# Performance work log

Hardware: AMD Instinct MI355X
Metric: run time of the kernel (lower is better)

## Reference

```python
import jax, jax.numpy as jnp
import numpy as np

N_NODES = 100000
N_EDGES = 1600000
IN_CH = 48
OUT_CH = 64
K = 2


def setup_inputs() -> dict:
    key = jax.random.key(0)
    k1, k2, k3, k4 = jax.random.split(key, 4)
    x = jax.random.normal(k1, (N_NODES, IN_CH), dtype=jnp.float32)
    edge_index = jax.random.randint(k2, (2, N_EDGES), 0, N_NODES, dtype=jnp.int64)
    W = jax.random.normal(k3, (IN_CH, OUT_CH), dtype=jnp.float32) * (1.0 / np.sqrt(IN_CH))
    b = jax.random.normal(k4, (OUT_CH,), dtype=jnp.float32) * 0.01
    return {"x": x, "edge_index": edge_index, "W": W, "b": b}


def _propagate(x, row, col):
    n = x.shape[0]
    # degree of each node counted over col (destination) indices
    deg = jax.ops.segment_sum(jnp.ones_like(col, dtype=x.dtype), col, num_segments=n)
    deg_inv_sqrt = jnp.where(deg > 0, jax.lax.rsqrt(jnp.where(deg > 0, deg, 1.0)), 0.0)
    norm = deg_inv_sqrt[row] * deg_inv_sqrt[col]  # [E]
    # gather-scale-scatter: out[col] += x[row] * norm
    msgs = x[row] * norm[:, None]  # [E, d]
    return jax.ops.segment_sum(msgs, col, num_segments=n)


def reference(x, edge_index, W, b):
    row, col = edge_index[0], edge_index[1]
    h = x
    for _ in range(K):
        h = _propagate(h, row, col)
    return h @ W + b
```

## Files before the change

kernel.cpp:

```cpp
#include <hip/hip_runtime.h>
#include <hip/hip_bf16.h>
#include <hip/hip_fp16.h>


#define N_NODES 100000
#define N_EDGES 1600000
#define IN_CH 48
#define OUT_CH 64
#define NBUCKETS 392
#define CAP 4608
#define EPB 2048
#define EPR 8
#define NBLK_EDGE 782
#define NBLK_BKT 391
#define RSTRIDE 32

__global__ void bucket_scatter_kernel(const int* __restrict__ row, const int* __restrict__ col,
                                      int* __restrict__ bucketCnt, int* __restrict__ edge_packed) {
    __shared__ int lh[NBUCKETS];
    __shared__ int lbase[NBUCKETS];
    __shared__ int rec[EPB];
    __shared__ unsigned short sbkt[EPB];
    int tid = threadIdx.x;
    int base = blockIdx.x * EPB;
    for (int i = tid; i < NBUCKETS; i += 256) lh[i] = 0;
    __syncthreads();
    #pragma unroll
    for (int k = 0; k < EPR; k++) {
        int e = base + k * 256 + tid;
        if (e < N_EDGES) {
            int c = col[e];
            int bkt = c >> 8;
            rec[k * 256 + tid] = (row[e] << 8) | (c & 255);
            sbkt[k * 256 + tid] = (unsigned short)bkt;
            atomicAdd(&lh[bkt], 1);
        }
    }
    __syncthreads();
    for (int i = tid; i < NBUCKETS; i += 256) {
        int c = lh[i];
        if (c > 0) lbase[i] = i * CAP + atomicAdd(&bucketCnt[i], c);
        lh[i] = 0;
    }
    __syncthreads();
    int total = min(EPB, N_EDGES - base);
    for (int i = tid; i < total; i += 256) {
        int bkt = sbkt[i];
        int p = atomicAdd(&lh[bkt], 1);
        int dst = lbase[bkt] + p;
        if (dst < (bkt + 1) * CAP)
            edge_packed[dst] = rec[i];
    }
}

__global__ void fine_sort_kernel(const int* __restrict__ edge_packed,
                                 const int* __restrict__ bucketCnt,
                                 int* __restrict__ edge_src,
                                 int* __restrict__ deg, int* __restrict__ start,
                                 float* __restrict__ dis, int* __restrict__ binTotal) {
    __shared__ int fh[256];
    __shared__ int cur[256];
    __shared__ int bh[64];
    __shared__ int wsum2[4];
    __shared__ int stage[CAP];
    int b = blockIdx.x;
    int t = threadIdx.x;
    int s0 = b * CAP;
    int n_edges = min(bucketCnt[b], CAP);
    int nodeBase = b << 8;
    if (t < 256) fh[t] = 0;
    if (t < 64) bh[t] = 0;
    __syncthreads();
    for (int j = t; j < n_edges; j += 512) {
        int rc = edge_packed[s0 + j];
        stage[j] = rc;
        atomicAdd(&fh[rc & 255], 1);
    }
    __syncthreads();
    if (t < 256) {
        int c = fh[t];
        int incl = c;
        int sl = t & 63, sw = t >> 6;
        #pragma unroll
        for (int o = 1; o < 64; o <<= 1) {
            int v = __shfl_up(incl, o, 64);
            if (sl >= o) incl += v;
        }
        if (sl == 63) wsum2[sw] = incl;
        __syncthreads();
        int wbase = 0;
        for (int k = 0; k < sw; k++) wbase += wsum2[k];
        incl += wbase;
        int ex = incl - c;
        int node = nodeBase + t;
        bool valid = (node < N_NODES);
        int d = c;
        float dv = (valid && d > 0) ? rsqrtf((float)d) : 0.0f;
        cur[t] = ex;
        if (valid) {
            deg[node] = d;
            start[node] = s0 + ex;
            dis[node] = dv;
            atomicAdd(&bh[min(d, 63)], 1);
        }
    } else {
        __syncthreads();
    }
    __syncthreads();
    for (int j = t; j < n_edges; j += 512) {
        int rc = stage[j];
        int p = atomicAdd(&cur[rc & 255], 1);
        edge_src[s0 + p] = rc >> 8;
    }
    __syncthreads();
    if (t < 64 && bh[t]) atomicAdd(&binTotal[t], bh[t]);
}

__global__ void scale_kernel(const float* __restrict__ x, const float* __restrict__ dis,
                             __half2* __restrict__ xs) {
    int g = blockIdx.x * 32 + (threadIdx.x >> 3);
    int c = (threadIdx.x & 7) * 3;
    float dd = dis[g];
    const float2* px = (const float2*)x + g * 24 + c;
    float2 v0 = px[0], v1 = px[1], v2 = px[2];
    __half2* q = xs + g * RSTRIDE + c;
    q[0] = __floats2half2_rn(v0.x * dd, v0.y * dd);
    q[1] = __floats2half2_rn(v1.x * dd, v1.y * dd);
    q[2] = __floats2half2_rn(v2.x * dd, v2.y * dd);
}

__global__ void order_kernel(const int* __restrict__ deg, const int* __restrict__ start,
                             const float* __restrict__ dis,
                             const int* __restrict__ binTotal, int* __restrict__ binCursor2,
                             int4* __restrict__ nodeinfo, int n) {
    __shared__ int lhist[64];
    __shared__ int lbase[64];
    int t = threadIdx.x;
    int i = blockIdx.x * 256 + t;
    if (t < 64) lhist[t] = 0;
    __syncthreads();
    int bin = 0, myrank = 0, d = 0;
    float dv = 0.0f;
    if (i < n) {
        d = deg[i];
        dv = dis[i];
        bin = min(d, 63);
        myrank = atomicAdd(&lhist[bin], 1);
    }
    __syncthreads();
    if (t < 64) {
        int c = binTotal[t];
        int incl = c;
        #pragma unroll
        for (int o = 1; o < 64; o <<= 1) {
            int v = __shfl_up(incl, o, 64);
            if (t >= o) incl += v;
        }
        int tot = __shfl(incl, 63, 64);
        int S = tot - incl;
        int add = (lhist[t] > 0) ? atomicAdd(&binCursor2[t], lhist[t]) : 0;
        lbase[t] = S + add;
    }
    __syncthreads();
    if (i < n)
        nodeinfo[lbase[bin] + myrank] = make_int4(i, start[i], d, __float_as_int(dv));
}

#define LOAD3(p, v0, v1, v2) { v0 = (p)[0]; v1 = (p)[1]; v2 = (p)[2]; }
#define ACC6(v0, v1, v2) { \
    float2 u0 = __half22float2(v0), u1 = __half22float2(v1), u2 = __half22float2(v2); \
    a0 += u0.x; a1 += u0.y; a2 += u1.x; a3 += u1.y; a4 += u2.x; a5 += u2.y; }
#define ACC6B(v0, v1, v2) { \
    float2 u0 = __half22float2(v0), u1 = __half22float2(v1), u2 = __half22float2(v2); \
    b0 += u0.x; b1 += u0.y; b2 += u1.x; b3 += u1.y; b4 += u2.x; b5 += u2.y; }

#define DECLD(P) __half2 P##00,P##01,P##02,P##10,P##11,P##12,P##20,P##21,P##22,P##30,P##31,P##32
#define DECLS(S) int S##0, S##1, S##2, S##3
#define LOADSRC(S) { S##0 = edge_src[j]; S##1 = edge_src[j+1]; \
                     S##2 = edge_src[j+2]; S##3 = edge_src[j+3]; j += 4; }
#define ISSUED(P, S, basep) { \
    const __half2* q0 = basep + S##0 * RSTRIDE + lane3; \
    const __half2* q1 = basep + S##1 * RSTRIDE + lane3; \
    const __half2* q2 = basep + S##2 * RSTRIDE + lane3; \
    const __half2* q3 = basep + S##3 * RSTRIDE + lane3; \
    P##00 = q0[0]; P##01 = q0[1]; P##02 = q0[2]; \
    P##10 = q1[0]; P##11 = q1[1]; P##12 = q1[2]; \
    P##20 = q2[0]; P##21 = q2[1]; P##22 = q2[2]; \
    P##30 = q3[0]; P##31 = q3[1]; P##32 = q3[2]; }
#define CONSUMED(P) { ACC6(P##00,P##01,P##02); ACC6B(P##10,P##11,P##12); \
                      ACC6(P##20,P##21,P##22); ACC6B(P##30,P##31,P##32); }

#define GATHER_PIPELINE(basep) { \
    int m = (e - s) >> 2; \
    DECLD(A); DECLD(B); \
    DECLS(sa); DECLS(sb); \
    if (m >= 2) { \
        LOADSRC(sa); LOADSRC(sb); \
        ISSUED(A, sa, basep); \
        m -= 2; \
        while (m >= 2) { \
            LOADSRC(sa); \
            ISSUED(B, sb, basep); \
            CONSUMED(A); \
            LOADSRC(sb); \
            ISSUED(A, sa, basep); \
            CONSUMED(B); \
            m -= 2; \
        } \
        if (m == 1) { \
            LOADSRC(sa); \
            ISSUED(B, sb, basep); \
            CONSUMED(A); \
            ISSUED(A, sa, basep); \
            CONSUMED(B); \
            CONSUMED(A); \
        } else { \
            ISSUED(B, sb, basep); \
            CONSUMED(A); \
            CONSUMED(B); \
        } \
    } else if (m == 1) { \
        LOADSRC(sa); \
        ISSUED(A, sa, basep); \
        CONSUMED(A); \
    } \
    for (; j < e; ++j) { \
        const __half2* p0 = basep + edge_src[j] * RSTRIDE + lane3; \
        __half2 v00, v01, v02; \
        LOAD3(p0, v00, v01, v02); \
        ACC6(v00, v01, v02); \
    } \
    a0 += b0; a1 += b1; a2 += b2; a3 += b3; a4 += b4; a5 += b5; }

__global__ void gather1_kernel(const __half2* __restrict__ xs,
                               const int* __restrict__ edge_src,
                               const int4* __restrict__ nodeinfo,
                               __half2* __restrict__ h1) {
    int g = blockIdx.x * 32 + (threadIdx.x >> 3);
    int lane3 = (threadIdx.x & 7) * 3;
    int4 ni = nodeinfo[g];
    int node = ni.x, s = ni.y, e = s + ni.z;
    float dv = __int_as_float(ni.w);
    float a0 = 0, a1 = 0, a2 = 0, a3 = 0, a4 = 0, a5 = 0;
    float b0 = 0, b1 = 0, b2 = 0, b3 = 0, b4 = 0, b5 = 0;
    int j = s;
    GATHER_PIPELINE(xs);
    float sc = dv * dv;
    __half2* q = h1 + node * RSTRIDE + lane3;
    q[0] = __floats2half2_rn(a0 * sc, a1 * sc);
    q[1] = __floats2half2_rn(a2 * sc, a3 * sc);
    q[2] = __floats2half2_rn(a4 * sc, a5 * sc);
}

__global__ void gather2_gemm_kernel(const __half2* __restrict__ h1,
                                    const int* __restrict__ edge_src,
                                    const int4* __restrict__ nodeinfo,
                                    const float* __restrict__ W,
                                    const float* __restrict__ bias,
                                    float* __restrict__ out) {
    __shared__ float sW[IN_CH * OUT_CH];
    __shared__ float sb[OUT_CH];
    __shared__ float sh[32][IN_CH + 1];

    for (int i = threadIdx.x; i < IN_CH * OUT_CH; i += 256) sW[i] = W[i];
    if (threadIdx.x < OUT_CH) sb[threadIdx.x] = bias[threadIdx.x];

    int nl = threadIdx.x >> 3;
    int lane = threadIdx.x & 7;
    int lane3 = lane * 3;
    int g = blockIdx.x * 32 + nl;
    int4 ni = nodeinfo[g];
    int node = ni.x, s = ni.y, e = s + ni.z;
    float dv = __int_as_float(ni.w);

    float a0 = 0, a1 = 0, a2 = 0, a3 = 0, a4 = 0, a5 = 0;
    float b0 = 0, b1 = 0, b2 = 0, b3 = 0, b4 = 0, b5 = 0;
    int j = s;
    GATHER_PIPELINE(h1);
    int c0 = 6 * lane;
    sh[nl][c0 + 0] = a0 * dv;
    sh[nl][c0 + 1] = a1 * dv;
    sh[nl][c0 + 2] = a2 * dv;
    sh[nl][c0 + 3] = a3 * dv;
    sh[nl][c0 + 4] = a4 * dv;
    sh[nl][c0 + 5] = a5 * dv;
    __syncthreads();

    int j0 = lane * 8;
    float acc[8];
    #pragma unroll
    for (int i = 0; i < 8; i++) acc[i] = sb[j0 + i];
    for (int k = 0; k < IN_CH; k++) {
        float s0 = sh[nl][k];
        #pragma unroll
        for (int i = 0; i < 8; i++) acc[i] += s0 * sW[k * OUT_CH + j0 + i];
    }
    float4* o = (float4*)(out + (size_t)node * OUT_CH + j0);
    o[0] = make_float4(acc[0], acc[1], acc[2], acc[3]);
    o[1] = make_float4(acc[4], acc[5], acc[6], acc[7]);
}

extern "C" void kernel_launch(void* const* d_in, const int* in_sizes, int n_in,
                              void* d_out, int out_size, void* d_ws, size_t ws_size,
                              hipStream_t stream) {
    const float* x   = (const float*)d_in[0];
    const int*   ei  = (const int*)d_in[1];
    const float* W   = (const float*)d_in[2];
    const float* b   = (const float*)d_in[3];
    float* out = (float*)d_out;

    const int* row = ei;
    const int* col = ei + N_EDGES;

    int* ws_i = (int*)d_ws;
    int* bucketCnt    = ws_i;
    int* binTotal     = ws_i + 512;
    int* binCursor2   = ws_i + 576;
    int* deg          = ws_i + 1024;
    int* start        = ws_i + 101376;
    float* dis        = (float*)(ws_i + 201728);
    int4* nodeinfo    = (int4*)(ws_i + 302080);
    int* edge_packed  = ws_i + 703488;
    __half2* xs       = (__half2*)(ws_i + 703488);
    int* edge_src     = ws_i + 3903488;
    __half2* h1       = (__half2*)(ws_i + 5709824);

    hipMemsetAsync(d_ws, 0, 640 * sizeof(int), stream);

    bucket_scatter_kernel<<<NBLK_EDGE, 256, 0, stream>>>(row, col, bucketCnt, edge_packed);
    fine_sort_kernel<<<NBLK_BKT, 512, 0, stream>>>(edge_packed, bucketCnt,
                                                   edge_src, deg, start, dis, binTotal);
    scale_kernel<<<N_NODES / 32, 256, 0, stream>>>(x, dis, xs);
    order_kernel<<<(N_NODES + 255) / 256, 256, 0, stream>>>(deg, start, dis, binTotal,
                                                            binCursor2, nodeinfo, N_NODES);

    gather1_kernel<<<N_NODES / 32, 256, 0, stream>>>(xs, edge_src, nodeinfo, h1);
    gather2_gemm_kernel<<<N_NODES / 32, 256, 0, stream>>>(h1, edge_src, nodeinfo, W, b, out);
}
```

Baseline: 206.1 us.

## Locally sort edges by bucket in shared memory before global scatter

The bucket scatter kernel now makes a histogram pass over col, prefix-scans the per-block bucket counts, and places each edge record into a bucket-sorted shared staging array. The final write loop then walks the staging array sequentially, so consecutive threads write to contiguous global positions within each bucket. This replaces the earlier scattered global writes with more coalesced ones. The cost is an extra read of col and one more scan with its barriers.

```diff
diff --git a/kernel.cpp b/kernel.cpp
--- a/kernel.cpp
+++ b/kernel.cpp
@@ -18,12 +18,48 @@
 __global__ void bucket_scatter_kernel(const int* __restrict__ row, const int* __restrict__ col,
                                       int* __restrict__ bucketCnt, int* __restrict__ edge_packed) {
     __shared__ int lh[NBUCKETS];
+    __shared__ int lofs[NBUCKETS];
     __shared__ int lbase[NBUCKETS];
-    __shared__ int rec[EPB];
+    __shared__ int stage[EPB];
     __shared__ unsigned short sbkt[EPB];
+    __shared__ int wsum[4];
     int tid = threadIdx.x;
     int base = blockIdx.x * EPB;
     for (int i = tid; i < NBUCKETS; i += 256) lh[i] = 0;
+    __syncthreads();
+    #pragma unroll
+    for (int k = 0; k < EPR; k++) {
+        int e = base + k * 256 + tid;
+        if (e < N_EDGES) atomicAdd(&lh[col[e] >> 8], 1);
+    }
+    __syncthreads();
+    {
+        int c0 = (tid < 196) ? lh[2 * tid] : 0;
+        int c1 = (tid < 196) ? lh[2 * tid + 1] : 0;
+        int s = c0 + c1;
+        int incl = s;
+        int lane = tid & 63, w = tid >> 6;
+        #pragma unroll
+        for (int o = 1; o < 64; o <<= 1) {
+            int v = __shfl_up(incl, o, 64);
+            if (lane >= o) incl += v;
+        }
+        if (lane == 63) wsum[w] = incl;
+        __syncthreads();
+        int wbase = 0;
+        for (int k = 0; k < w; k++) wbase += wsum[k];
+        int ex = wbase + incl - s;
+        if (tid < 196) {
+            lofs[2 * tid]     = ex;
+            lofs[2 * tid + 1] = ex + c0;
+        }
+    }
+    __syncthreads();
+    for (int i = tid; i < NBUCKETS; i += 256) {
+        int c = lh[i];
+        if (c > 0) lbase[i] = i * CAP + atomicAdd(&bucketCnt[i], c);
+        lh[i] = 0;
+    }
     __syncthreads();
     #pragma unroll
     for (int k = 0; k < EPR; k++) {
@@ -31,25 +67,19 @@
         if (e < N_EDGES) {
             int c = col[e];
             int bkt = c >> 8;
-            rec[k * 256 + tid] = (row[e] << 8) | (c & 255);
-            sbkt[k * 256 + tid] = (unsigned short)bkt;
-            atomicAdd(&lh[bkt], 1);
-        }
-    }
-    __syncthreads();
-    for (int i = tid; i < NBUCKETS; i += 256) {
-        int c = lh[i];
-        if (c > 0) lbase[i] = i * CAP + atomicAdd(&bucketCnt[i], c);
-        lh[i] = 0;
-    }
-    __syncthreads();
-    int total = min(EPB, N_EDGES - base);
+            int r = atomicAdd(&lh[bkt], 1);
+            int slot = lofs[bkt] + r;
+            stage[slot] = (row[e] << 8) | (c & 255);
+            sbkt[slot] = (unsigned short)bkt;
+        }
+    }
+    __syncthreads();
+    int total = (base + EPB <= N_EDGES) ? EPB : (N_EDGES - base);
     for (int i = tid; i < total; i += 256) {
         int bkt = sbkt[i];
-        int p = atomicAdd(&lh[bkt], 1);
-        int dst = lbase[bkt] + p;
+        int dst = lbase[bkt] + (i - lofs[bkt]);
         if (dst < (bkt + 1) * CAP)
-            edge_packed[dst] = rec[i];
+            edge_packed[dst] = stage[i];
     }
 }
 
```

Measured after the change: 206.0 us (median of 2 runs). No clear change (-0.1%).
